# Kernel tuning notes

Measured on AMD Instinct MI355X. Metric: run time of the kernel, lower is better.

The kernel has to match this reference:

```python
import jax, jax.numpy as jnp
import numpy as np

BETA = 0.5
PS = 4  # threshold rank per row, and pooling ratio N//PS


def _getM(att, ps):
    # att: [B, N]. Per-row descending sort; threshold = (ps+1)-th largest value.
    vals = -jnp.sort(-att, axis=1)            # descending sort, [B, N]
    thr = vals[:, ps, None]                   # [B, 1]
    mask = att >= thr                         # [B, N] bool
    return jnp.sum(mask.astype(att.dtype), axis=0)  # [N] counts


def setup_inputs() -> dict:
    key = jax.random.key(0)
    k1, k2, k3, k4 = jax.random.split(key, 4)
    B, N, D = 64, 2048, 512
    return {
        "x": jax.random.normal(k1, (B, N, D), dtype=jnp.float32),
        "y": jax.random.normal(k2, (B, N, N), dtype=jnp.float32),
        "attention": jax.random.normal(k3, (B, N), dtype=jnp.float32),
        "att_off": jax.random.normal(k4, (B, N), dtype=jnp.float32),
    }


def reference(x, y, attention, att_off):
    # attention is already [B, N]; flatten(start_dim=1) is a no-op here.
    M = BETA * _getM(attention, PS) + (1.0 - BETA) * _getM(att_off, PS)  # [N]
    # torch.sort(descending=True) on M; take top N//ps indices.
    top_m = jnp.argsort(-M)[: M.shape[0] // PS]  # [K], K = N//PS
    x_sel = x[:, top_m]                          # [B, K, D]
    y_sel = y[:, top_m][:, :, top_m]             # [B, K, K] (two-stage gather)
    return (x_sel, y_sel, top_m)
```

## Files before the change

### kernel.cpp

```cpp
#include <hip/hip_runtime.h>
#include <math.h>

#define NN 2048
#define BB 64
#define DD 512
#define NSEL 512

typedef float fx4 __attribute__((ext_vector_type(4)));

__device__ __forceinline__ void insert5(float v, float t[5]) {
  if (v > t[4]) {
    if (v > t[0])      { t[4]=t[3]; t[3]=t[2]; t[2]=t[1]; t[1]=t[0]; t[0]=v; }
    else if (v > t[1]) { t[4]=t[3]; t[3]=t[2]; t[2]=t[1]; t[1]=v; }
    else if (v > t[2]) { t[4]=t[3]; t[3]=t[2]; t[2]=v; }
    else if (v > t[3]) { t[4]=t[3]; t[3]=v; }
    else               { t[4]=v; }
  }
}

__global__ void thr_kernel(const float* __restrict__ att,
                           const float* __restrict__ aoff,
                           float* __restrict__ thr) {
  int blk  = blockIdx.x;
  const float* src = (blk < BB) ? att : aoff;
  int row  = (blk < BB) ? blk : blk - BB;
  int lane = threadIdx.x;

  float t[5] = {-INFINITY, -INFINITY, -INFINITY, -INFINITY, -INFINITY};
  const float* rp = src + (size_t)row * NN;
  #pragma unroll
  for (int k = 0; k < NN / 64; ++k) insert5(rp[lane + 64 * k], t);

  for (int off = 1; off < 64; off <<= 1) {
    float b[5];
    #pragma unroll
    for (int k = 0; k < 5; ++k) b[k] = __shfl_xor(t[k], off, 64);
    float m[5];
    int ia = 0, ib = 0;
    #pragma unroll
    for (int k = 0; k < 5; ++k) {
      float av = t[ia], bv = b[ib];
      bool ta = (av >= bv);
      m[k] = ta ? av : bv;
      ia += ta ? 1 : 0;
      ib += ta ? 0 : 1;
    }
    #pragma unroll
    for (int k = 0; k < 5; ++k) t[k] = m[k];
  }
  if (lane == 0) thr[blk] = t[4];
}

__global__ void mkey_kernel(const float* __restrict__ att,
                            const float* __restrict__ aoff,
                            const float* __restrict__ thr,
                            int* __restrict__ key) {
  int n = blockIdx.x * 64 + threadIdx.x;
  if (n >= NN) return;
  int c = 0;
  #pragma unroll 16
  for (int b = 0; b < BB; ++b) c += (att[(size_t)b * NN + n] >= thr[b]) ? 1 : 0;
  #pragma unroll 16
  for (int b = 0; b < BB; ++b) c += (aoff[(size_t)b * NN + n] >= thr[BB + b]) ? 1 : 0;
  key[n] = c;
}

__global__ void __launch_bounds__(1024)
topm_kernel(const int* __restrict__ key,
            int* __restrict__ top_m,
            float* __restrict__ out_tail) {
  __shared__ int kl[NN];
  __shared__ int chist[32][132];
  __shared__ int htot[132];
  __shared__ int gbase[132];
  int t = threadIdx.x;

  for (int i = t; i < 32 * 132; i += 1024) (&chist[0][0])[i] = 0;
  __syncthreads();

  int k0 = key[t];
  int k1 = key[t + 1024];
  kl[t] = k0;
  kl[t + 1024] = k1;
  int c0 = t >> 6;
  int c1 = 16 + (t >> 6);
  atomicAdd(&chist[c0][k0], 1);
  atomicAdd(&chist[c1][k1], 1);
  __syncthreads();

  if (t < 129) {
    int run = 0;
    #pragma unroll 4
    for (int c = 0; c < 32; ++c) { int v = chist[c][t]; chist[c][t] = run; run += v; }
    htot[t] = run;
  }
  __syncthreads();
  if (t == 0) {
    int acc = 0;
    for (int k = 128; k >= 0; --k) { gbase[k] = acc; acc += htot[k]; }
  }
  __syncthreads();

  int n0 = t, n1 = t + 1024;
  int pre0 = 0;
  for (int j = c0 * 64; j < n0; ++j) pre0 += (kl[j] == k0) ? 1 : 0;
  int pre1 = 0;
  for (int j = c1 * 64; j < n1; ++j) pre1 += (kl[j] == k1) ? 1 : 0;

  int r0 = gbase[k0] + chist[c0][k0] + pre0;
  int r1 = gbase[k1] + chist[c1][k1] + pre1;
  if (r0 < NSEL) { top_m[r0] = n0; out_tail[r0] = (float)n0; }
  if (r1 < NSEL) { top_m[r1] = n1; out_tail[r1] = (float)n1; }
}

__global__ void __launch_bounds__(256)
gather_kernel(const float* __restrict__ x,
              const float* __restrict__ y,
              const int* __restrict__ top_m,
              float* __restrict__ xs,
              float* __restrict__ ys) {
  __shared__ float rowbuf[4][NN];
  __shared__ int cols[NSEL];
  int t = threadIdx.x;
  int w = t >> 6, lane = t & 63;
  int blk = blockIdx.x;
  int b = blk >> 4;
  int iblk = blk & 15;

  cols[t]       = top_m[t];
  cols[t + 256] = top_m[t + 256];
  __syncthreads();

  float* myrow = rowbuf[w];
  int i0 = iblk * 32 + w * 8;
  const float* ybase = y + (size_t)b * NN * NN;

  fx4 pr[8];
  {
    int r = cols[i0];
    const fx4* src = (const fx4*)(ybase + (size_t)r * NN);
    #pragma unroll
    for (int j = 0; j < 8; ++j)
      pr[j] = __builtin_nontemporal_load(&src[lane + 64 * j]);
  }

  #pragma unroll
  for (int k = 0; k < 8; ++k) {
    int i = i0 + k;
    {
      fx4* mb = (fx4*)myrow;
      #pragma unroll
      for (int j = 0; j < 8; ++j) mb[lane + 64 * j] = pr[j];
    }
    if (k < 7) {
      int rn = cols[i + 1];
      const fx4* src = (const fx4*)(ybase + (size_t)rn * NN);
      #pragma unroll
      for (int j = 0; j < 8; ++j)
        pr[j] = __builtin_nontemporal_load(&src[lane + 64 * j]);
    }
    {
      int r = cols[i];
      const fx4* xsrc = (const fx4*)(x + ((size_t)b * NN + r) * DD);
      fx4*       xdst = (fx4*)(xs + ((size_t)b * NSEL + i) * DD);
      #pragma unroll
      for (int j = 0; j < 2; ++j) {
        fx4 v = __builtin_nontemporal_load(&xsrc[lane + 64 * j]);
        __builtin_nontemporal_store(v, &xdst[lane + 64 * j]);
      }
    }
    {
      float o[8];
      #pragma unroll
      for (int j = 0; j < 8; ++j) o[j] = myrow[cols[8 * lane + j]];
      fx4* dst = (fx4*)(ys + ((size_t)b * NSEL + i) * DD);
      fx4 o0 = {o[0], o[1], o[2], o[3]};
      fx4 o1 = {o[4], o[5], o[6], o[7]};
      __builtin_nontemporal_store(o0, &dst[2 * lane]);
      __builtin_nontemporal_store(o1, &dst[2 * lane + 1]);
    }
  }
}

extern "C" void kernel_launch(void* const* d_in, const int* in_sizes, int n_in,
                              void* d_out, int out_size, void* d_ws, size_t ws_size,
                              hipStream_t stream) {
  const float* x    = (const float*)d_in[0];
  const float* y    = (const float*)d_in[1];
  const float* att  = (const float*)d_in[2];
  const float* aoff = (const float*)d_in[3];

  float* out = (float*)d_out;
  float* xs   = out;
  float* ysel = out + (size_t)BB * NSEL * DD;
  float* tail = ysel + (size_t)BB * NSEL * NSEL;

  float* thr   = (float*)d_ws;
  int*   key   = (int*)d_ws + 128;
  int*   top_m = (int*)d_ws + 128 + NN;

  hipLaunchKernelGGL(thr_kernel, dim3(2 * BB), dim3(64), 0, stream, att, aoff, thr);
  hipLaunchKernelGGL(mkey_kernel, dim3(32), dim3(64), 0, stream, att, aoff, thr, key);
  hipLaunchKernelGGL(topm_kernel, dim3(1), dim3(1024), 0, stream, key, top_m, tail);
  hipLaunchKernelGGL(gather_kernel, dim3(BB * 16), dim3(256), 0, stream,
                     x, y, top_m, xs, ysel);
}
```

Before: 129.8 us.

## Fuse threshold, key and top-m kernels into one block; double-buffer y row prefetch

Merges the three small prep kernels (per-row threshold, per-column count, ranking) into a single 1024-thread block, which removes two launches and the global round trips for thresholds and keys. The cost is that all 128 row thresholds are now computed serially by 16 waves on one CU rather than by 128 blocks. Separately, the gather kernel keeps two y rows in flight with A/B register buffers instead of one, to hide more memory latency at the price of extra registers.

```diff
diff --git a/kernel.cpp b/kernel.cpp
--- a/kernel.cpp
+++ b/kernel.cpp
@@ -18,74 +18,65 @@
   }
 }
 
-__global__ void thr_kernel(const float* __restrict__ att,
-                           const float* __restrict__ aoff,
-                           float* __restrict__ thr) {
-  int blk  = blockIdx.x;
-  const float* src = (blk < BB) ? att : aoff;
-  int row  = (blk < BB) ? blk : blk - BB;
-  int lane = threadIdx.x;
-
-  float t[5] = {-INFINITY, -INFINITY, -INFINITY, -INFINITY, -INFINITY};
-  const float* rp = src + (size_t)row * NN;
-  #pragma unroll
-  for (int k = 0; k < NN / 64; ++k) insert5(rp[lane + 64 * k], t);
-
-  for (int off = 1; off < 64; off <<= 1) {
-    float b[5];
-    #pragma unroll
-    for (int k = 0; k < 5; ++k) b[k] = __shfl_xor(t[k], off, 64);
-    float m[5];
-    int ia = 0, ib = 0;
-    #pragma unroll
-    for (int k = 0; k < 5; ++k) {
-      float av = t[ia], bv = b[ib];
-      bool ta = (av >= bv);
-      m[k] = ta ? av : bv;
-      ia += ta ? 1 : 0;
-      ib += ta ? 0 : 1;
-    }
-    #pragma unroll
-    for (int k = 0; k < 5; ++k) t[k] = m[k];
-  }
-  if (lane == 0) thr[blk] = t[4];
-}
-
-__global__ void mkey_kernel(const float* __restrict__ att,
-                            const float* __restrict__ aoff,
-                            const float* __restrict__ thr,
-                            int* __restrict__ key) {
-  int n = blockIdx.x * 64 + threadIdx.x;
-  if (n >= NN) return;
-  int c = 0;
-  #pragma unroll 16
-  for (int b = 0; b < BB; ++b) c += (att[(size_t)b * NN + n] >= thr[b]) ? 1 : 0;
-  #pragma unroll 16
-  for (int b = 0; b < BB; ++b) c += (aoff[(size_t)b * NN + n] >= thr[BB + b]) ? 1 : 0;
-  key[n] = c;
-}
-
 __global__ void __launch_bounds__(1024)
-topm_kernel(const int* __restrict__ key,
+prep_kernel(const float* __restrict__ att,
+            const float* __restrict__ aoff,
             int* __restrict__ top_m,
             float* __restrict__ out_tail) {
+  __shared__ float thr_s[128];
   __shared__ int kl[NN];
   __shared__ int chist[32][132];
   __shared__ int htot[132];
   __shared__ int gbase[132];
   int t = threadIdx.x;
+  int w = t >> 6, lane = t & 63;
 
   for (int i = t; i < 32 * 132; i += 1024) (&chist[0][0])[i] = 0;
-  __syncthreads();
-
-  int k0 = key[t];
-  int k1 = key[t + 1024];
-  kl[t] = k0;
-  kl[t + 1024] = k1;
-  int c0 = t >> 6;
-  int c1 = 16 + (t >> 6);
-  atomicAdd(&chist[c0][k0], 1);
-  atomicAdd(&chist[c1][k1], 1);
+
+  for (int q = 0; q < 8; ++q) {
+    int r = w * 8 + q;
+    const float* rp = (r < BB) ? (att + (size_t)r * NN)
+                               : (aoff + (size_t)(r - BB) * NN);
+    float tt[5] = {-INFINITY, -INFINITY, -INFINITY, -INFINITY, -INFINITY};
+    #pragma unroll
+    for (int k = 0; k < NN / 64; ++k) insert5(rp[lane + 64 * k], tt);
+
+    for (int off = 1; off < 64; off <<= 1) {
+      float bb[5];
+      #pragma unroll
+      for (int k = 0; k < 5; ++k) bb[k] = __shfl_xor(tt[k], off, 64);
+      float m[5];
+      int ia = 0, ib = 0;
+      #pragma unroll
+      for (int k = 0; k < 5; ++k) {
+        float av = tt[ia], bv = bb[ib];
+        bool ta = (av >= bv);
+        m[k] = ta ? av : bv;
+        ia += ta ? 1 : 0;
+        ib += ta ? 0 : 1;
+      }
+      #pragma unroll
+      for (int k = 0; k < 5; ++k) tt[k] = m[k];
+    }
+    if (lane == 0) thr_s[r] = tt[4];
+  }
+  __syncthreads();
+
+  int c0 = t, c1 = t + 1024;
+  int k0 = 0, k1 = 0;
+  #pragma unroll 8
+  for (int b = 0; b < BB; ++b) {
+    float ta = thr_s[b], to = thr_s[BB + b];
+    k0 += (att [(size_t)b * NN + c0] >= ta) ? 1 : 0;
+    k0 += (aoff[(size_t)b * NN + c0] >= to) ? 1 : 0;
+    k1 += (att [(size_t)b * NN + c1] >= ta) ? 1 : 0;
+    k1 += (aoff[(size_t)b * NN + c1] >= to) ? 1 : 0;
+  }
+  kl[c0] = k0;
+  kl[c1] = k1;
+  int ch0 = t >> 6, ch1 = 16 + (t >> 6);
+  atomicAdd(&chist[ch0][k0], 1);
+  atomicAdd(&chist[ch1][k1], 1);
   __syncthreads();
 
   if (t < 129) {
@@ -103,15 +94,51 @@
 
   int n0 = t, n1 = t + 1024;
   int pre0 = 0;
-  for (int j = c0 * 64; j < n0; ++j) pre0 += (kl[j] == k0) ? 1 : 0;
+  for (int j = ch0 * 64; j < n0; ++j) pre0 += (kl[j] == k0) ? 1 : 0;
   int pre1 = 0;
-  for (int j = c1 * 64; j < n1; ++j) pre1 += (kl[j] == k1) ? 1 : 0;
-
-  int r0 = gbase[k0] + chist[c0][k0] + pre0;
-  int r1 = gbase[k1] + chist[c1][k1] + pre1;
+  for (int j = ch1 * 64; j < n1; ++j) pre1 += (kl[j] == k1) ? 1 : 0;
+
+  int r0 = gbase[k0] + chist[ch0][k0] + pre0;
+  int r1 = gbase[k1] + chist[ch1][k1] + pre1;
   if (r0 < NSEL) { top_m[r0] = n0; out_tail[r0] = (float)n0; }
   if (r1 < NSEL) { top_m[r1] = n1; out_tail[r1] = (float)n1; }
 }
+
+#define ROW_STEP(K, PR)                                                        \
+  do {                                                                         \
+    int i_ = i0 + (K);                                                         \
+    {                                                                          \
+      fx4* mb_ = (fx4*)myrow;                                                  \
+      _Pragma("unroll")                                                        \
+      for (int j = 0; j < 8; ++j) mb_[lane + 64 * j] = PR[j];                  \
+    }                                                                          \
+    if ((K) + 2 < 8) {                                                         \
+      const fx4* s_ = (const fx4*)(ybase + (size_t)cols[i_ + 2] * NN);         \
+      _Pragma("unroll")                                                        \
+      for (int j = 0; j < 8; ++j)                                              \
+        PR[j] = __builtin_nontemporal_load(&s_[lane + 64 * j]);                \
+    }                                                                          \
+    {                                                                          \
+      int r_ = cols[i_];                                                       \
+      const fx4* xsrc_ = (const fx4*)(x + ((size_t)b * NN + r_) * DD);         \
+      fx4*       xdst_ = (fx4*)(xs + ((size_t)b * NSEL + i_) * DD);            \
+      _Pragma("unroll")                                                        \
+      for (int j = 0; j < 2; ++j) {                                            \
+        fx4 v_ = __builtin_nontemporal_load(&xsrc_[lane + 64 * j]);            \
+        __builtin_nontemporal_store(v_, &xdst_[lane + 64 * j]);                \
+      }                                                                        \
+    }                                                                          \
+    {                                                                          \
+      float o_[8];                                                             \
+      _Pragma("unroll")                                                        \
+      for (int j = 0; j < 8; ++j) o_[j] = myrow[cols[8 * lane + j]];           \
+      fx4* dst_ = (fx4*)(ys + ((size_t)b * NSEL + i_) * DD);                   \
+      fx4 o0_ = {o_[0], o_[1], o_[2], o_[3]};                                  \
+      fx4 o1_ = {o_[4], o_[5], o_[6], o_[7]};                                  \
+      __builtin_nontemporal_store(o0_, &dst_[2 * lane]);                       \
+      __builtin_nontemporal_store(o1_, &dst_[2 * lane + 1]);                   \
+    }                                                                          \
+  } while (0)
 
 __global__ void __launch_bounds__(256)
 gather_kernel(const float* __restrict__ x,
@@ -135,50 +162,22 @@
   int i0 = iblk * 32 + w * 8;
   const float* ybase = y + (size_t)b * NN * NN;
 
-  fx4 pr[8];
+  fx4 prA[8], prB[8];
   {
-    int r = cols[i0];
-    const fx4* src = (const fx4*)(ybase + (size_t)r * NN);
+    const fx4* sA = (const fx4*)(ybase + (size_t)cols[i0] * NN);
     #pragma unroll
     for (int j = 0; j < 8; ++j)
-      pr[j] = __builtin_nontemporal_load(&src[lane + 64 * j]);
+      prA[j] = __builtin_nontemporal_load(&sA[lane + 64 * j]);
+    const fx4* sB = (const fx4*)(ybase + (size_t)cols[i0 + 1] * NN);
+    #pragma unroll
+    for (int j = 0; j < 8; ++j)
+      prB[j] = __builtin_nontemporal_load(&sB[lane + 64 * j]);
   }
 
   #pragma unroll
-  for (int k = 0; k < 8; ++k) {
-    int i = i0 + k;
-    {
-      fx4* mb = (fx4*)myrow;
-      #pragma unroll
-      for (int j = 0; j < 8; ++j) mb[lane + 64 * j] = pr[j];
-    }
-    if (k < 7) {
-      int rn = cols[i + 1];
-      const fx4* src = (const fx4*)(ybase + (size_t)rn * NN);
-      #pragma unroll
-      for (int j = 0; j < 8; ++j)
-        pr[j] = __builtin_nontemporal_load(&src[lane + 64 * j]);
-    }
-    {
-      int r = cols[i];
-      const fx4* xsrc = (const fx4*)(x + ((size_t)b * NN + r) * DD);
-      fx4*       xdst = (fx4*)(xs + ((size_t)b * NSEL + i) * DD);
-      #pragma unroll
-      for (int j = 0; j < 2; ++j) {
-        fx4 v = __builtin_nontemporal_load(&xsrc[lane + 64 * j]);
-        __builtin_nontemporal_store(v, &xdst[lane + 64 * j]);
-      }
-    }
-    {
-      float o[8];
-      #pragma unroll
-      for (int j = 0; j < 8; ++j) o[j] = myrow[cols[8 * lane + j]];
-      fx4* dst = (fx4*)(ys + ((size_t)b * NSEL + i) * DD);
-      fx4 o0 = {o[0], o[1], o[2], o[3]};
-      fx4 o1 = {o[4], o[5], o[6], o[7]};
-      __builtin_nontemporal_store(o0, &dst[2 * lane]);
-      __builtin_nontemporal_store(o1, &dst[2 * lane + 1]);
-    }
+  for (int kk = 0; kk < 4; ++kk) {
+    ROW_STEP(2 * kk,     prA);
+    ROW_STEP(2 * kk + 1, prB);
   }
 }
 
@@ -195,13 +194,10 @@
   float* ysel = out + (size_t)BB * NSEL * DD;
   float* tail = ysel + (size_t)BB * NSEL * NSEL;
 
-  float* thr   = (float*)d_ws;
-  int*   key   = (int*)d_ws + 128;
-  int*   top_m = (int*)d_ws + 128 + NN;
-
-  hipLaunchKernelGGL(thr_kernel, dim3(2 * BB), dim3(64), 0, stream, att, aoff, thr);
-  hipLaunchKernelGGL(mkey_kernel, dim3(32), dim3(64), 0, stream, att, aoff, thr, key);
-  hipLaunchKernelGGL(topm_kernel, dim3(1), dim3(1024), 0, stream, key, top_m, tail);
+  int* top_m = (int*)d_ws;
+
+  hipLaunchKernelGGL(prep_kernel, dim3(1), dim3(1024), 0, stream,
+                     att, aoff, top_m, tail);
   hipLaunchKernelGGL(gather_kernel, dim3(BB * 16), dim3(256), 0, stream,
                      x, y, top_m, xs, ysel);
 }
```

New measurement: 185.9 us. 43.2% more time.

## Fuse threshold and key kernels; recompute top-m ranking inside each gather block

Applied to the files above, without the earlier changes.

Merges the per-row threshold and count kernels into one prep kernel in which every block redundantly computes all 128 thresholds and then counts its own 64 columns. The single-block top-m ranking kernel is removed, and each of the 1024 gather blocks now recomputes the full stable counting-sort ranking in shared memory, reusing the row-buffer space through a union. The aim is to cut two kernel launches and their serialization gaps. The cost is 32-fold redundant threshold work and 1024-fold redundant ranking work ahead of every gather, including a serial prefix scan done by one thread.

```diff
diff --git a/kernel.cpp b/kernel.cpp
--- a/kernel.cpp
+++ b/kernel.cpp
@@ -18,120 +18,125 @@
   }
 }
 
-__global__ void thr_kernel(const float* __restrict__ att,
-                           const float* __restrict__ aoff,
-                           float* __restrict__ thr) {
-  int blk  = blockIdx.x;
-  const float* src = (blk < BB) ? att : aoff;
-  int row  = (blk < BB) ? blk : blk - BB;
-  int lane = threadIdx.x;
-
-  float t[5] = {-INFINITY, -INFINITY, -INFINITY, -INFINITY, -INFINITY};
-  const float* rp = src + (size_t)row * NN;
-  #pragma unroll
-  for (int k = 0; k < NN / 64; ++k) insert5(rp[lane + 64 * k], t);
-
-  for (int off = 1; off < 64; off <<= 1) {
-    float b[5];
-    #pragma unroll
-    for (int k = 0; k < 5; ++k) b[k] = __shfl_xor(t[k], off, 64);
-    float m[5];
-    int ia = 0, ib = 0;
-    #pragma unroll
-    for (int k = 0; k < 5; ++k) {
-      float av = t[ia], bv = b[ib];
-      bool ta = (av >= bv);
-      m[k] = ta ? av : bv;
-      ia += ta ? 1 : 0;
-      ib += ta ? 0 : 1;
-    }
-    #pragma unroll
-    for (int k = 0; k < 5; ++k) t[k] = m[k];
-  }
-  if (lane == 0) thr[blk] = t[4];
-}
-
-__global__ void mkey_kernel(const float* __restrict__ att,
-                            const float* __restrict__ aoff,
-                            const float* __restrict__ thr,
-                            int* __restrict__ key) {
-  int n = blockIdx.x * 64 + threadIdx.x;
-  if (n >= NN) return;
+__global__ void __launch_bounds__(256)
+prep_kernel(const float* __restrict__ att,
+            const float* __restrict__ aoff,
+            int* __restrict__ key_g) {
+  __shared__ float thr_s[128];
+  int t = threadIdx.x;
+  int w = t >> 6, lane = t & 63;
+
+  for (int q = 0; q < 32; ++q) {
+    int r = w * 32 + q;
+    const float* rp = (r < BB) ? (att + (size_t)r * NN)
+                               : (aoff + (size_t)(r - BB) * NN);
+    float tt[5] = {-INFINITY, -INFINITY, -INFINITY, -INFINITY, -INFINITY};
+    #pragma unroll
+    for (int k = 0; k < NN / 64; ++k) insert5(rp[lane + 64 * k], tt);
+
+    for (int off = 1; off < 64; off <<= 1) {
+      float bb[5];
+      #pragma unroll
+      for (int k = 0; k < 5; ++k) bb[k] = __shfl_xor(tt[k], off, 64);
+      float m[5];
+      int ia = 0, ib = 0;
+      #pragma unroll
+      for (int k = 0; k < 5; ++k) {
+        float av = tt[ia], bv = bb[ib];
+        bool ta = (av >= bv);
+        m[k] = ta ? av : bv;
+        ia += ta ? 1 : 0;
+        ib += ta ? 0 : 1;
+      }
+      #pragma unroll
+      for (int k = 0; k < 5; ++k) tt[k] = m[k];
+    }
+    if (lane == 0) thr_s[r] = tt[4];
+  }
+  __syncthreads();
+
+  int col = blockIdx.x * 64 + (t >> 2);
+  int seg = t & 3;
   int c = 0;
-  #pragma unroll 16
-  for (int b = 0; b < BB; ++b) c += (att[(size_t)b * NN + n] >= thr[b]) ? 1 : 0;
-  #pragma unroll 16
-  for (int b = 0; b < BB; ++b) c += (aoff[(size_t)b * NN + n] >= thr[BB + b]) ? 1 : 0;
-  key[n] = c;
-}
-
-__global__ void __launch_bounds__(1024)
-topm_kernel(const int* __restrict__ key,
-            int* __restrict__ top_m,
-            float* __restrict__ out_tail) {
-  __shared__ int kl[NN];
-  __shared__ int chist[32][132];
-  __shared__ int htot[132];
-  __shared__ int gbase[132];
-  int t = threadIdx.x;
-
-  for (int i = t; i < 32 * 132; i += 1024) (&chist[0][0])[i] = 0;
-  __syncthreads();
-
-  int k0 = key[t];
-  int k1 = key[t + 1024];
-  kl[t] = k0;
-  kl[t + 1024] = k1;
-  int c0 = t >> 6;
-  int c1 = 16 + (t >> 6);
-  atomicAdd(&chist[c0][k0], 1);
-  atomicAdd(&chist[c1][k1], 1);
-  __syncthreads();
-
-  if (t < 129) {
-    int run = 0;
-    #pragma unroll 4
-    for (int c = 0; c < 32; ++c) { int v = chist[c][t]; chist[c][t] = run; run += v; }
-    htot[t] = run;
-  }
-  __syncthreads();
-  if (t == 0) {
-    int acc = 0;
-    for (int k = 128; k >= 0; --k) { gbase[k] = acc; acc += htot[k]; }
-  }
-  __syncthreads();
-
-  int n0 = t, n1 = t + 1024;
-  int pre0 = 0;
-  for (int j = c0 * 64; j < n0; ++j) pre0 += (kl[j] == k0) ? 1 : 0;
-  int pre1 = 0;
-  for (int j = c1 * 64; j < n1; ++j) pre1 += (kl[j] == k1) ? 1 : 0;
-
-  int r0 = gbase[k0] + chist[c0][k0] + pre0;
-  int r1 = gbase[k1] + chist[c1][k1] + pre1;
-  if (r0 < NSEL) { top_m[r0] = n0; out_tail[r0] = (float)n0; }
-  if (r1 < NSEL) { top_m[r1] = n1; out_tail[r1] = (float)n1; }
-}
+  #pragma unroll 8
+  for (int b = seg * 32; b < seg * 32 + 32; ++b) {
+    float v = (b < BB) ? att[(size_t)b * NN + col]
+                       : aoff[(size_t)(b - BB) * NN + col];
+    c += (v >= thr_s[b]) ? 1 : 0;
+  }
+  c += __shfl_down(c, 1, 64);
+  c += __shfl_down(c, 2, 64);
+  if (seg == 0) key_g[col] = c;
+}
+
+struct SortS {
+  int kl[NN];
+  int chist[32][132];
+  int htot[132];
+  int gbase[132];
+};
+struct GatherS {
+  float rowbuf[4][NN];
+};
 
 __global__ void __launch_bounds__(256)
 gather_kernel(const float* __restrict__ x,
               const float* __restrict__ y,
-              const int* __restrict__ top_m,
+              const int* __restrict__ key_g,
               float* __restrict__ xs,
-              float* __restrict__ ys) {
-  __shared__ float rowbuf[4][NN];
+              float* __restrict__ ys,
+              float* __restrict__ tail) {
   __shared__ int cols[NSEL];
+  __shared__ union { SortS s; GatherS g; } sm;
   int t = threadIdx.x;
   int w = t >> 6, lane = t & 63;
-  int blk = blockIdx.x;
-  int b = blk >> 4;
-  int iblk = blk & 15;
-
-  cols[t]       = top_m[t];
-  cols[t + 256] = top_m[t + 256];
-  __syncthreads();
-
-  float* myrow = rowbuf[w];
+  int bk = blockIdx.x;
+  int b = bk >> 4;
+  int iblk = bk & 15;
+
+  {
+    int* flat = &sm.s.chist[0][0];
+    for (int i = t; i < 32 * 132; i += 256) flat[i] = 0;
+    __syncthreads();
+    int myk[8];
+    #pragma unroll
+    for (int p = 0; p < 8; ++p) {
+      int n = t + 256 * p;
+      int k = key_g[n];
+      sm.s.kl[n] = k;
+      myk[p] = k;
+      atomicAdd(&sm.s.chist[n >> 6][k], 1);
+    }
+    __syncthreads();
+    if (t < 129) {
+      int run = 0;
+      #pragma unroll 4
+      for (int c = 0; c < 32; ++c) { int v = sm.s.chist[c][t]; sm.s.chist[c][t] = run; run += v; }
+      sm.s.htot[t] = run;
+    }
+    __syncthreads();
+    if (t == 0) {
+      int acc = 0;
+      for (int k = 128; k >= 0; --k) { sm.s.gbase[k] = acc; acc += sm.s.htot[k]; }
+    }
+    __syncthreads();
+    #pragma unroll
+    for (int p = 0; p < 8; ++p) {
+      int n = t + 256 * p;
+      int k = myk[p];
+      int c = n >> 6;
+      int pre = 0;
+      for (int j = c * 64; j < n; ++j) pre += (sm.s.kl[j] == k) ? 1 : 0;
+      int r = sm.s.gbase[k] + sm.s.chist[c][k] + pre;
+      if (r < NSEL) {
+        cols[r] = n;
+        if (bk == 0) tail[r] = (float)n;
+      }
+    }
+    __syncthreads();
+  }
+
+  float* myrow = sm.g.rowbuf[w];
   int i0 = iblk * 32 + w * 8;
   const float* ybase = y + (size_t)b * NN * NN;
 
@@ -190,18 +195,15 @@
   const float* att  = (const float*)d_in[2];
   const float* aoff = (const float*)d_in[3];
 
-  float* out = (float*)d_out;
+  float* out  = (float*)d_out;
   float* xs   = out;
   float* ysel = out + (size_t)BB * NSEL * DD;
   float* tail = ysel + (size_t)BB * NSEL * NSEL;
 
-  float* thr   = (float*)d_ws;
-  int*   key   = (int*)d_ws + 128;
-  int*   top_m = (int*)d_ws + 128 + NN;
-
-  hipLaunchKernelGGL(thr_kernel, dim3(2 * BB), dim3(64), 0, stream, att, aoff, thr);
-  hipLaunchKernelGGL(mkey_kernel, dim3(32), dim3(64), 0, stream, att, aoff, thr, key);
-  hipLaunchKernelGGL(topm_kernel, dim3(1), dim3(1024), 0, stream, key, top_m, tail);
+  int* key_g = (int*)d_ws;
+
+  hipLaunchKernelGGL(prep_kernel, dim3(32), dim3(256), 0, stream,
+                     att, aoff, key_g);
   hipLaunchKernelGGL(gather_kernel, dim3(BB * 16), dim3(256), 0, stream,
-                     x, y, top_m, xs, ysel);
-}
+                     x, y, key_g, xs, ysel, tail);
+}
```

Result: slower. 375.3 us (+189.1%).

## Parallelize top-m ranking with wave scans and ballot match; branchless top-5 insert

Applied to the files above, without the earlier changes.

The threshold kernel now loads rows as float4 and uses a branchless fmax/fmin insertion network to track the top five values. In the single-block ranking kernel, the serial per-key column prefix and the single-thread global base loop are replaced with shuffle-based wave scans. The O(64) per-thread linear count of equal keys is replaced with an 8-bit ballot match plus popcount. These changes target latency in the small serial pre-gather kernels. The gather kernel, which handles most of the memory traffic, is unchanged, so the overall effect is limited to the small-kernel share of total time.

```diff
diff --git a/kernel.cpp b/kernel.cpp
--- a/kernel.cpp
+++ b/kernel.cpp
@@ -8,14 +8,13 @@
 
 typedef float fx4 __attribute__((ext_vector_type(4)));
 
-__device__ __forceinline__ void insert5(float v, float t[5]) {
-  if (v > t[4]) {
-    if (v > t[0])      { t[4]=t[3]; t[3]=t[2]; t[2]=t[1]; t[1]=t[0]; t[0]=v; }
-    else if (v > t[1]) { t[4]=t[3]; t[3]=t[2]; t[2]=t[1]; t[1]=v; }
-    else if (v > t[2]) { t[4]=t[3]; t[3]=t[2]; t[2]=v; }
-    else if (v > t[3]) { t[4]=t[3]; t[3]=v; }
-    else               { t[4]=v; }
-  }
+__device__ __forceinline__ void insert5b(float v, float t[5]) {
+  float a = v, m;
+  m = fmaxf(t[0], a); a = fminf(t[0], a); t[0] = m;
+  m = fmaxf(t[1], a); a = fminf(t[1], a); t[1] = m;
+  m = fmaxf(t[2], a); a = fminf(t[2], a); t[2] = m;
+  m = fmaxf(t[3], a); a = fminf(t[3], a); t[3] = m;
+  t[4] = fmaxf(t[4], a);
 }
 
 __global__ void thr_kernel(const float* __restrict__ att,
@@ -27,9 +26,12 @@
   int lane = threadIdx.x;
 
   float t[5] = {-INFINITY, -INFINITY, -INFINITY, -INFINITY, -INFINITY};
-  const float* rp = src + (size_t)row * NN;
+  const fx4* rp4 = (const fx4*)(src + (size_t)row * NN);
   #pragma unroll
-  for (int k = 0; k < NN / 64; ++k) insert5(rp[lane + 64 * k], t);
+  for (int k = 0; k < NN / 256; ++k) {
+    fx4 v = rp4[lane + 64 * k];
+    insert5b(v.x, t); insert5b(v.y, t); insert5b(v.z, t); insert5b(v.w, t);
+  }
 
   for (int off = 1; off < 64; off <<= 1) {
     float b[5];
@@ -69,48 +71,82 @@
 topm_kernel(const int* __restrict__ key,
             int* __restrict__ top_m,
             float* __restrict__ out_tail) {
-  __shared__ int kl[NN];
   __shared__ int chist[32][132];
   __shared__ int htot[132];
   __shared__ int gbase[132];
   int t = threadIdx.x;
+  int w = t >> 6, lane = t & 63;
 
   for (int i = t; i < 32 * 132; i += 1024) (&chist[0][0])[i] = 0;
   __syncthreads();
 
   int k0 = key[t];
   int k1 = key[t + 1024];
-  kl[t] = k0;
-  kl[t + 1024] = k1;
-  int c0 = t >> 6;
-  int c1 = 16 + (t >> 6);
-  atomicAdd(&chist[c0][k0], 1);
-  atomicAdd(&chist[c1][k1], 1);
-  __syncthreads();
-
-  if (t < 129) {
-    int run = 0;
-    #pragma unroll 4
-    for (int c = 0; c < 32; ++c) { int v = chist[c][t]; chist[c][t] = run; run += v; }
-    htot[t] = run;
-  }
-  __syncthreads();
-  if (t == 0) {
-    int acc = 0;
-    for (int k = 128; k >= 0; --k) { gbase[k] = acc; acc += htot[k]; }
-  }
-  __syncthreads();
-
-  int n0 = t, n1 = t + 1024;
-  int pre0 = 0;
-  for (int j = c0 * 64; j < n0; ++j) pre0 += (kl[j] == k0) ? 1 : 0;
-  int pre1 = 0;
-  for (int j = c1 * 64; j < n1; ++j) pre1 += (kl[j] == k1) ? 1 : 0;
-
-  int r0 = gbase[k0] + chist[c0][k0] + pre0;
-  int r1 = gbase[k1] + chist[c1][k1] + pre1;
-  if (r0 < NSEL) { top_m[r0] = n0; out_tail[r0] = (float)n0; }
-  if (r1 < NSEL) { top_m[r1] = n1; out_tail[r1] = (float)n1; }
+  atomicAdd(&chist[w][k0], 1);
+  atomicAdd(&chist[16 + w][k1], 1);
+  __syncthreads();
+
+  {
+    int c = lane & 31;
+    #pragma unroll
+    for (int rd = 0; rd < 5; ++rd) {
+      int kb = rd * 32 + w * 2 + (lane >> 5);
+      if (kb <= 128) {
+        int v = chist[c][kb];
+        int inc = v;
+        #pragma unroll
+        for (int d = 1; d < 32; d <<= 1) {
+          int o = __shfl_up(inc, d, 32);
+          if (c >= d) inc += o;
+        }
+        chist[c][kb] = inc - v;
+        if (c == 31) htot[kb] = inc;
+      }
+    }
+  }
+  __syncthreads();
+
+  if (t < 64) {
+    int carry = 0;
+    #pragma unroll
+    for (int rd = 0; rd < 3; ++rd) {
+      int k = 128 - (rd * 64 + lane);
+      int v = (k >= 0) ? htot[k] : 0;
+      int inc = v;
+      #pragma unroll
+      for (int d = 1; d < 64; d <<= 1) {
+        int o = __shfl_up(inc, d, 64);
+        if (lane >= d) inc += o;
+      }
+      if (k >= 0) gbase[k] = carry + inc - v;
+      carry += __shfl(inc, 63, 64);
+    }
+  }
+  __syncthreads();
+
+  unsigned long long lt = (lane == 0) ? 0ull : (~0ull >> (64 - lane));
+  {
+    unsigned long long m = ~0ull;
+    #pragma unroll
+    for (int bit = 0; bit < 8; ++bit) {
+      unsigned long long bb = __ballot(((k0 >> bit) & 1) != 0);
+      m &= ((k0 >> bit) & 1) ? bb : ~bb;
+    }
+    int pre0 = __popcll(m & lt);
+    int r0 = gbase[k0] + chist[w][k0] + pre0;
+    if (r0 < NSEL) { top_m[r0] = t; out_tail[r0] = (float)t; }
+  }
+  {
+    unsigned long long m = ~0ull;
+    #pragma unroll
+    for (int bit = 0; bit < 8; ++bit) {
+      unsigned long long bb = __ballot(((k1 >> bit) & 1) != 0);
+      m &= ((k1 >> bit) & 1) ? bb : ~bb;
+    }
+    int pre1 = __popcll(m & lt);
+    int r1 = gbase[k1] + chist[16 + w][k1] + pre1;
+    if (r1 < NSEL) { top_m[r1] = t + 1024; out_tail[r1] = (float)(t + 1024); }
+  }
 }
 
 __global__ void __launch_bounds__(256)
@@ -190,7 +226,7 @@
   const float* att  = (const float*)d_in[2];
   const float* aoff = (const float*)d_in[3];
 
-  float* out = (float*)d_out;
+  float* out  = (float*)d_out;
   float* xs   = out;
   float* ysel = out + (size_t)BB * NSEL * DD;
   float* tail = ysel + (size_t)BB * NSEL * NSEL;
```

Result: faster. 121.8 us, median of 2 (-6.2%).
